# Optimization experiments

Measured on AMD Instinct MI355X. Metric: run time of the kernel, lower is better.

## Reference

```python
import jax, jax.numpy as jnp
import numpy as np

SEQ_LEN = 2048
D_MODEL = 1024
K = 32
B = 16
CP = K * (K + 1) // 2  # 528


def _spectral_filters(seq_len: int, k: int) -> np.ndarray:
    # Hankel matrix Z_ij = 2 / ((i+j)^3 - (i+j)), 1-indexed
    e = np.arange(1, seq_len + 1, dtype=np.float64)
    ipj = e[:, None] + e[None, :]
    Z = 2.0 / (ipj ** 3 - ipj)
    sigma, phi = np.linalg.eigh(Z)
    sk = np.clip(sigma[-k:], 1e-9, None)
    return (phi[:, -k:] * sk ** 0.25).astype(np.float32)


# static upper-triangular index pattern and sqrt(2) off-diagonal scaling
_IU0, _IU1 = np.triu_indices(K)
_SCALE = np.where(_IU0 == _IU1, 1.0, np.sqrt(2.0)).astype(np.float32)


def setup_inputs() -> dict:
    key = jax.random.key(0)
    ks = jax.random.split(key, 8)
    filters = jnp.asarray(_spectral_filters(SEQ_LEN, K))
    x = jax.random.normal(ks[0], (B, SEQ_LEN, D_MODEL), dtype=jnp.float32)
    pre_w = jax.random.normal(ks[1], (SEQ_LEN, D_MODEL), dtype=jnp.float32) / np.sqrt(D_MODEL)
    pre_b = jnp.zeros((SEQ_LEN,), dtype=jnp.float32)
    qp_w = jax.random.normal(ks[2], (CP, K), dtype=jnp.float32) / np.sqrt(K)
    qp_b = jnp.zeros((CP,), dtype=jnp.float32)
    o_w = jax.random.normal(ks[3], (D_MODEL, CP), dtype=jnp.float32) / np.sqrt(CP)
    o_b = jnp.zeros((D_MODEL,), dtype=jnp.float32)
    decay = jnp.ones((SEQ_LEN,), dtype=jnp.float32)
    return {
        'x': x,
        'pre_w': pre_w, 'pre_b': pre_b,
        'q_filters': filters,          # learnable copy
        'k_filters': filters,          # fixed buffer copy
        'qp_w': qp_w, 'qp_b': qp_b,
        'o_w': o_w, 'o_b': o_b,
        'decay': decay,
    }


def reference(x, pre_w, pre_b, q_filters, k_filters, qp_w, qp_b, o_w, o_b, decay):
    # pre_proj: (B,T,d_model) -> (B,T,seq_len)
    x_proj = x @ pre_w.T + pre_b
    # spectral projections onto top-K filters: (B,T,K)
    Q = jnp.einsum('bti,ik->btk', x_proj, q_filters)
    Q = Q @ qp_w.T + qp_b                      # (B,T,CP)
    V = jnp.einsum('bti,ik->btk', x_proj, k_filters)
    # symmetric outer product compressed to upper triangle, off-diag * sqrt(2)
    iu0 = jnp.asarray(_IU0)
    iu1 = jnp.asarray(_IU1)
    scale = jnp.asarray(_SCALE)
    Z = V[..., iu0] * V[..., iu1] * scale      # (B,T,CP), avoids (B,T,K,K)
    Z = Z * decay[None, :, None]
    H = jnp.cumsum(Z, axis=1)                  # causal state accumulation
    Y = Q * H
    return Y @ o_w.T + o_b                     # (B,T,d_model)
```

## Files before the change

### kernel.cpp

```cpp
#include <hip/hip_runtime.h>
#include <hip/hip_bf16.h>
#include <math.h>

#define T_SEQ   2048
#define DM      1024
#define KF      32
#define BATCH   16
#define CPDIM   528
#define KPAD    576
#define MROWS   (BATCH * T_SEQ)
#define NCHUNK  32
#define TCHUNK  64

typedef __bf16 bf16x8 __attribute__((ext_vector_type(8)));
typedef float f32x4 __attribute__((ext_vector_type(4)));
typedef unsigned uint2v __attribute__((ext_vector_type(2)));

__device__ __forceinline__ unsigned packsplit(float v) {
  unsigned u = __float_as_uint(v);
  unsigned h = (u + 0x7fffu + ((u >> 16) & 1u)) & 0xffff0000u;
  float rr = v - __uint_as_float(h);
  return h | (__float_as_uint(rr) >> 16);
}

__device__ __forceinline__ unsigned short f2bf(float f) {
  unsigned u = __float_as_uint(f);
  return (unsigned short)((u + 0x7fffu + ((u >> 16) & 1u)) >> 16);
}

__device__ __forceinline__ void gload16(const void* g, void* l) {
  __builtin_amdgcn_global_load_lds(
      (const __attribute__((address_space(1))) unsigned*)g,
      (__attribute__((address_space(3))) unsigned*)l, 16, 0, 0);
}

__global__ __launch_bounds__(256) void k_fold_part(const float* __restrict__ pre_w,
                                                   const float* __restrict__ qf,
                                                   const float* __restrict__ kfil,
                                                   float* __restrict__ Wp) {
  const int sc = blockIdx.x;
  const int it = blockIdx.y;
  const int s0 = sc * 64, i0 = it * 64;
  const int tid = threadIdx.x;
  __shared__ float fs[64][64];
  __shared__ float ps[64][64];
  for (int idx = tid; idx < 4096; idx += 256) {
    const int s = idx >> 6, c = idx & 63;
    fs[s][c] = (c < KF) ? qf[(s0 + s) * KF + c] : kfil[(s0 + s) * KF + c - KF];
    ps[s][c] = pre_w[(size_t)(s0 + s) * DM + i0 + c];
  }
  __syncthreads();
  const int i = tid & 63;
  const int kb = tid >> 6;
  float acc[16] = {};
  for (int s = 0; s < 64; ++s) {
    const float pv = ps[s][i];
    const float4 f0 = *reinterpret_cast<const float4*>(&fs[s][kb * 16 + 0]);
    const float4 f1 = *reinterpret_cast<const float4*>(&fs[s][kb * 16 + 4]);
    const float4 f2 = *reinterpret_cast<const float4*>(&fs[s][kb * 16 + 8]);
    const float4 f3 = *reinterpret_cast<const float4*>(&fs[s][kb * 16 + 12]);
    acc[0]  = fmaf(pv, f0.x, acc[0]);  acc[1]  = fmaf(pv, f0.y, acc[1]);
    acc[2]  = fmaf(pv, f0.z, acc[2]);  acc[3]  = fmaf(pv, f0.w, acc[3]);
    acc[4]  = fmaf(pv, f1.x, acc[4]);  acc[5]  = fmaf(pv, f1.y, acc[5]);
    acc[6]  = fmaf(pv, f1.z, acc[6]);  acc[7]  = fmaf(pv, f1.w, acc[7]);
    acc[8]  = fmaf(pv, f2.x, acc[8]);  acc[9]  = fmaf(pv, f2.y, acc[9]);
    acc[10] = fmaf(pv, f2.z, acc[10]); acc[11] = fmaf(pv, f2.w, acc[11]);
    acc[12] = fmaf(pv, f3.x, acc[12]); acc[13] = fmaf(pv, f3.y, acc[13]);
    acc[14] = fmaf(pv, f3.z, acc[14]); acc[15] = fmaf(pv, f3.w, acc[15]);
  }
#pragma unroll
  for (int j = 0; j < 16; ++j)
    Wp[((size_t)sc * 64 + kb * 16 + j) * DM + i0 + i] = acc[j];
}

__global__ __launch_bounds__(256) void k_foldred(const float* __restrict__ Wp,
                                                 unsigned short* __restrict__ Wt_hi,
                                                 unsigned short* __restrict__ Wt_lo) {
  const int idx = blockIdx.x * 256 + threadIdx.x;
  float acc = 0.f;
#pragma unroll
  for (int sc = 0; sc < NCHUNK; ++sc)
    acc += Wp[(size_t)sc * 64 * DM + idx];
  const unsigned pk = packsplit(acc);
  Wt_hi[idx] = (unsigned short)(pk >> 16);
  Wt_lo[idx] = (unsigned short)(pk & 0xffffu);
}

__global__ __launch_bounds__(256) void k_bias(const float* __restrict__ pre_b,
                                              const float* __restrict__ qf,
                                              const float* __restrict__ kfil,
                                              float* __restrict__ bias64) {
  __shared__ float part[4][64];
  const int k = threadIdx.x & 63;
  const int q = threadIdx.x >> 6;
  float acc = 0.f;
  for (int s = q * 512; s < (q + 1) * 512; ++s) {
    const float fv = (k < KF) ? qf[s * KF + k] : kfil[s * KF + k - KF];
    acc = fmaf(pre_b[s], fv, acc);
  }
  part[q][k] = acc;
  __syncthreads();
  if (threadIdx.x < 64)
    bias64[threadIdx.x] = part[0][k] + part[1][k] + part[2][k] + part[3][k];
}

__global__ __launch_bounds__(256) void k_q0v(const float* __restrict__ x,
                                             const unsigned short* __restrict__ Wt_hi,
                                             const unsigned short* __restrict__ Wt_lo,
                                             const float* __restrict__ bias64,
                                             float* __restrict__ Q0V) {
  __shared__ float Xs[2][64 * 32];
  __shared__ unsigned short Wh[2][64 * 32];
  __shared__ unsigned short Wl[2][64 * 32];
  const int tid = threadIdx.x;
  const int m0 = blockIdx.x * 64;
  const int w = tid >> 6, l = tid & 63;
  const int g = l >> 4, r = l & 15;

  f32x4 acc[4] = {};

  auto stage = [&](int buf, int k0) {
#pragma unroll
    for (int q = 0; q < 2; ++q) {
      const int c = q * 256 + tid;
      const int row = c >> 3, sl = c & 7;
      const int col4 = (sl ^ (row & 7)) * 4;
      gload16(&x[(size_t)(m0 + row) * DM + k0 + col4], &Xs[buf][c * 4]);
    }
    {
      const int row = tid >> 2, sl = tid & 3;
      const int colh = (sl ^ ((row >> 1) & 3)) * 8;
      gload16(&Wt_hi[(size_t)row * DM + k0 + colh], &Wh[buf][tid * 8]);
      gload16(&Wt_lo[(size_t)row * DM + k0 + colh], &Wl[buf][tid * 8]);
    }
  };

  stage(0, 0);
  for (int it = 0; it < DM / 32; ++it) {
    const int cur = it & 1;
    __syncthreads();
    if (it + 1 < DM / 32) stage(cur ^ 1, (it + 1) * 32);

    const int arow = w * 16 + r;
    const int sx = (2 * g) ^ (arow & 7);
    const int sy = (2 * g + 1) ^ (arow & 7);
    const f32x4 pX = *reinterpret_cast<const f32x4*>(&Xs[cur][arow * 32 + sx * 4]);
    const f32x4 pY = *reinterpret_cast<const f32x4*>(&Xs[cur][arow * 32 + sy * 4]);
    unsigned pk[8];
#pragma unroll
    for (int e = 0; e < 4; ++e) { pk[e] = packsplit(pX[e]); pk[4 + e] = packsplit(pY[e]); }
    union { unsigned u[4]; bf16x8 v; } ah, al;
#pragma unroll
    for (int j = 0; j < 4; ++j) {
      ah.u[j] = (pk[2 * j] >> 16) | (pk[2 * j + 1] & 0xffff0000u);
      al.u[j] = (pk[2 * j] & 0xffffu) | (pk[2 * j + 1] << 16);
    }

    bf16x8 bh[4], bl[4];
#pragma unroll
    for (int n = 0; n < 4; ++n) {
      const int brow = n * 16 + r;
      const int bs = g ^ ((brow >> 1) & 3);
      const int off = brow * 32 + bs * 8;
      bh[n] = *reinterpret_cast<const bf16x8*>(&Wh[cur][off]);
      bl[n] = *reinterpret_cast<const bf16x8*>(&Wl[cur][off]);
    }
#pragma unroll
    for (int n = 0; n < 4; ++n) {
      acc[n] = __builtin_amdgcn_mfma_f32_16x16x32_bf16(bh[n], ah.v, acc[n], 0, 0, 0);
      acc[n] = __builtin_amdgcn_mfma_f32_16x16x32_bf16(bh[n], al.v, acc[n], 0, 0, 0);
      acc[n] = __builtin_amdgcn_mfma_f32_16x16x32_bf16(bl[n], ah.v, acc[n], 0, 0, 0);
    }
  }
  const int row_o = m0 + w * 16 + r;
#pragma unroll
  for (int n = 0; n < 4; ++n) {
    const int col_o = n * 16 + g * 4;
    const float4 bb = *reinterpret_cast<const float4*>(&bias64[col_o]);
    float4 v;
    v.x = acc[n][0] + bb.x; v.y = acc[n][1] + bb.y;
    v.z = acc[n][2] + bb.z; v.w = acc[n][3] + bb.w;
    *reinterpret_cast<float4*>(&Q0V[(size_t)row_o * 64 + col_o]) = v;
  }
}

__global__ __launch_bounds__(576) void k_chunksum(const float* __restrict__ Q0V,
                                                  const float* __restrict__ decay,
                                                  float* __restrict__ S) {
  const int ch = blockIdx.x;
  const int b  = blockIdx.y;
  __shared__ float vs[TCHUNK * KF];
  __shared__ float dec[TCHUNK];
  const int tid = threadIdx.x;
  const int t0 = ch * TCHUNK;

  for (int idx = tid; idx < TCHUNK * KF; idx += 576) {
    const int t = idx >> 5, j = idx & 31;
    vs[idx] = Q0V[(size_t)(b * T_SEQ + t0 + t) * 64 + KF + j];
  }
  if (tid < TCHUNK) dec[tid] = decay[t0 + tid];
  __syncthreads();

  if (tid >= CPDIM) return;
  const int c = tid;
  int i = 0, rem = c;
  while (rem >= KF - i) { rem -= KF - i; ++i; }
  const int j = i + rem;
  const float sc = (i == j) ? 1.0f : 1.41421356237309515f;
  float h = 0.f;
#pragma unroll 4
  for (int t = 0; t < TCHUNK; ++t)
    h = fmaf(vs[t * KF + i] * vs[t * KF + j], dec[t], h);
  S[(size_t)(b * NCHUNK + ch) * CPDIM + c] = h * sc;
}

__global__ __launch_bounds__(576) void k_scanchunks(float* __restrict__ S) {
  const int b = blockIdx.x;
  const int c = threadIdx.x;
  if (c >= CPDIM) return;
  float v[NCHUNK];
#pragma unroll
  for (int ch = 0; ch < NCHUNK; ++ch)
    v[ch] = S[(size_t)(b * NCHUNK + ch) * CPDIM + c];
  float run = 0.f;
#pragma unroll
  for (int ch = 0; ch < NCHUNK; ++ch) {
    S[(size_t)(b * NCHUNK + ch) * CPDIM + c] = run;
    run += v[ch];
  }
}

__global__ __launch_bounds__(576) void k_scan_y(const float* __restrict__ Q0V,
                                                const float* __restrict__ S,
                                                const float* __restrict__ qp_w,
                                                const float* __restrict__ qp_b,
                                                const float* __restrict__ decay,
                                                unsigned short* __restrict__ Yb) {
  const int ch = blockIdx.x;
  const int b  = blockIdx.y;
  __shared__ float vs[TCHUNK * KF];
  __shared__ float qs[TCHUNK * KF];
  __shared__ float dec[TCHUNK];
  const int tid = threadIdx.x;
  const int t0 = ch * TCHUNK;

  for (int idx = tid; idx < TCHUNK * KF; idx += 576) {
    const int t = idx >> 5, j = idx & 31;
    const size_t row = (size_t)(b * T_SEQ + t0 + t) * 64;
    qs[idx] = Q0V[row + j];
    vs[idx] = Q0V[row + KF + j];
  }
  if (tid < TCHUNK) dec[tid] = decay[t0 + tid];
  __syncthreads();

  const int c = tid;
  if (c >= CPDIM) {
    for (int t = 0; t < TCHUNK; ++t)
      Yb[(size_t)(b * T_SEQ + t0 + t) * KPAD + c] = 0;
    return;
  }
  int i = 0, rem = c;
  while (rem >= KF - i) { rem -= KF - i; ++i; }
  const int j = i + rem;
  const float sc = (i == j) ? 1.0f : 1.41421356237309515f;

  float w[KF];
#pragma unroll
  for (int q = 0; q < KF; ++q) w[q] = qp_w[c * KF + q];
  const float qb = qp_b[c];

  float h = S[(size_t)(b * NCHUNK + ch) * CPDIM + c];
  for (int t = 0; t < TCHUNK; ++t) {
    const float z = vs[t * KF + i] * vs[t * KF + j] * sc * dec[t];
    h += z;
    float qv = qb;
#pragma unroll
    for (int q = 0; q < KF; ++q) qv = fmaf(w[q], qs[t * KF + q], qv);
    Yb[(size_t)(b * T_SEQ + t0 + t) * KPAD + c] = f2bf(qv * h);
  }
}

__global__ __launch_bounds__(256) void k_owb(const float* __restrict__ ow,
                                             unsigned short* __restrict__ owb) {
  const int idx = blockIdx.x * 256 + threadIdx.x;
  if (idx >= DM * KPAD) return;
  const int n = idx / KPAD, k = idx - n * KPAD;
  owb[idx] = (k < CPDIM) ? f2bf(ow[(size_t)n * CPDIM + k]) : (unsigned short)0;
}

__global__ __launch_bounds__(256) void k_out_mfma(const unsigned short* __restrict__ Yb,
                                                  const unsigned short* __restrict__ owb,
                                                  const float* __restrict__ ob,
                                                  float* __restrict__ out) {
  __shared__ unsigned short As[128 * 64];
  __shared__ unsigned short Bs[128 * 64];

  const int wg = blockIdx.x;
  const int nb = (wg & 7) * 256 + (wg >> 3);
  const int m0 = (nb >> 3) * 128;
  const int n0 = (nb & 7) * 128;

  const int tid = threadIdx.x;
  const int w = tid >> 6, l = tid & 63;
  const int wr = w >> 1, wc = w & 1;
  const int g = l >> 4, r = l & 15;

  f32x4 acc[4][4] = {};

  auto stage = [&](int k0) {
#pragma unroll
    for (int i = 0; i < 4; ++i) {
      const int c = i * 256 + tid;
      const int row = c >> 3, colh = (c & 7) * 8;
      gload16(&Yb [(size_t)(m0 + row) * KPAD + k0 + colh], &As[c * 8]);
      gload16(&owb[(size_t)(n0 + row) * KPAD + k0 + colh], &Bs[c * 8]);
    }
  };

  stage(0);
  for (int it = 0; it < KPAD / 64; ++it) {
    __syncthreads();

#pragma unroll
    for (int ksub = 0; ksub < 2; ++ksub) {
      bf16x8 af[4], bf[4];
      const int kh = ksub * 32 + g * 8;
#pragma unroll
      for (int m = 0; m < 4; ++m)
        af[m] = *reinterpret_cast<const bf16x8*>(&As[(wr * 64 + m * 16 + r) * 64 + kh]);
#pragma unroll
      for (int n = 0; n < 4; ++n)
        bf[n] = *reinterpret_cast<const bf16x8*>(&Bs[(wc * 64 + n * 16 + r) * 64 + kh]);
#pragma unroll
      for (int m = 0; m < 4; ++m)
#pragma unroll
        for (int n = 0; n < 4; ++n)
          acc[m][n] = __builtin_amdgcn_mfma_f32_16x16x32_bf16(bf[n], af[m], acc[m][n], 0, 0, 0);
    }

    __syncthreads();
    if (it + 1 < KPAD / 64) stage((it + 1) * 64);
  }

#pragma unroll
  for (int m = 0; m < 4; ++m) {
    const int row_o = m0 + wr * 64 + m * 16 + r;
#pragma unroll
    for (int n = 0; n < 4; ++n) {
      const int col_o = n0 + wc * 64 + n * 16 + g * 4;
      const float4 bb = *reinterpret_cast<const float4*>(&ob[col_o]);
      float4 v;
      v.x = acc[m][n][0] + bb.x; v.y = acc[m][n][1] + bb.y;
      v.z = acc[m][n][2] + bb.z; v.w = acc[m][n][3] + bb.w;
      *reinterpret_cast<float4*>(&out[(size_t)row_o * DM + col_o]) = v;
    }
  }
}

extern "C" void kernel_launch(void* const* d_in, const int* in_sizes, int n_in,
                              void* d_out, int out_size, void* d_ws, size_t ws_size,
                              hipStream_t stream) {
  const float* x      = (const float*)d_in[0];
  const float* pre_w  = (const float*)d_in[1];
  const float* pre_b  = (const float*)d_in[2];
  const float* q_filt = (const float*)d_in[3];
  const float* k_filt = (const float*)d_in[4];
  const float* qp_w   = (const float*)d_in[5];
  const float* qp_b   = (const float*)d_in[6];
  const float* o_w    = (const float*)d_in[7];
  const float* o_b    = (const float*)d_in[8];
  const float* decay  = (const float*)d_in[9];
  float* out = (float*)d_out;

  char* ws = (char*)d_ws;
  unsigned short* Wt_hi = (unsigned short*)(ws);
  unsigned short* Wt_lo = (unsigned short*)(ws + 131072);
  float*    bias64 = (float*)(ws + 262144);
  float*    Q0V    = (float*)(ws + 262400);
  unsigned short* owb = (unsigned short*)(ws + 262400);
  float*    S      = (float*)(ws + 8651008);
  unsigned short* Yb = (unsigned short*)(ws + 9732352);
  float*    Wp     = (float*)(ws + 50331648);

  k_fold_part<<<dim3(NCHUNK, 16), dim3(256), 0, stream>>>(pre_w, q_filt, k_filt, Wp);
  k_foldred<<<dim3(256), dim3(256), 0, stream>>>(Wp, Wt_hi, Wt_lo);
  k_bias<<<dim3(1), dim3(256), 0, stream>>>(pre_b, q_filt, k_filt, bias64);
  k_q0v<<<dim3(MROWS / 64), dim3(256), 0, stream>>>(x, Wt_hi, Wt_lo, bias64, Q0V);
  k_chunksum<<<dim3(NCHUNK, BATCH), dim3(576), 0, stream>>>(Q0V, decay, S);
  k_scanchunks<<<dim3(BATCH), dim3(576), 0, stream>>>(S);
  k_scan_y<<<dim3(NCHUNK, BATCH), dim3(576), 0, stream>>>(Q0V, S, qp_w, qp_b, decay, Yb);
  k_owb<<<dim3((DM * KPAD + 255) / 256), dim3(256), 0, stream>>>(o_w, owb);
  k_out_mfma<<<dim3((MROWS / 128) * (DM / 128)), dim3(256), 0, stream>>>(Yb, owb, o_b, out);
}
```

Before: 205.2 us.

## Fuse chunk sums into Q0V GEMM and scan_y into output GEMM via LDS

Merges the bias reduction into the fold-reduce kernel and computes per-chunk state sums inside the Q0V projection kernel from values already in registers. It also fuses the intra-chunk scan and Y computation into the output GEMM: each 64-row block builds its bf16 Y tile in LDS (padded stride) and multiplies it by o_w fragments loaded straight from global memory into registers with double buffering. This removes the global Yb round trip and several launches, and trims the K padding from 576 to 544. In exchange the output GEMM block covers the full 1024-wide N with large register accumulators and reads B from global memory without LDS staging, which may hurt occupancy and bandwidth.

Result: slower. 219.9 us (+7.2%).

```diff
diff --git a/kernel.cpp b/kernel.cpp
--- a/kernel.cpp
+++ b/kernel.cpp
@@ -7,7 +7,8 @@
 #define KF      32
 #define BATCH   16
 #define CPDIM   528
-#define KPAD    576
+#define KPAD    544
+#define YSTR    552
 #define MROWS   (BATCH * T_SEQ)
 #define NCHUNK  32
 #define TCHUNK  64
@@ -73,9 +74,28 @@
     Wp[((size_t)sc * 64 + kb * 16 + j) * DM + i0 + i] = acc[j];
 }
 
-__global__ __launch_bounds__(256) void k_foldred(const float* __restrict__ Wp,
-                                                 unsigned short* __restrict__ Wt_hi,
-                                                 unsigned short* __restrict__ Wt_lo) {
+__global__ __launch_bounds__(256) void k_foldred_bias(const float* __restrict__ Wp,
+                                                      const float* __restrict__ pre_b,
+                                                      const float* __restrict__ qf,
+                                                      const float* __restrict__ kfil,
+                                                      unsigned short* __restrict__ Wt_hi,
+                                                      unsigned short* __restrict__ Wt_lo,
+                                                      float* __restrict__ bias64) {
+  if (blockIdx.x == 256) {
+    __shared__ float part[4][64];
+    const int k = threadIdx.x & 63;
+    const int q = threadIdx.x >> 6;
+    float acc = 0.f;
+    for (int s = q * 512; s < (q + 1) * 512; ++s) {
+      const float fv = (k < KF) ? qf[s * KF + k] : kfil[s * KF + k - KF];
+      acc = fmaf(pre_b[s], fv, acc);
+    }
+    part[q][k] = acc;
+    __syncthreads();
+    if (threadIdx.x < 64)
+      bias64[threadIdx.x] = part[0][k] + part[1][k] + part[2][k] + part[3][k];
+    return;
+  }
   const int idx = blockIdx.x * 256 + threadIdx.x;
   float acc = 0.f;
 #pragma unroll
@@ -86,32 +106,18 @@
   Wt_lo[idx] = (unsigned short)(pk & 0xffffu);
 }
 
-__global__ __launch_bounds__(256) void k_bias(const float* __restrict__ pre_b,
-                                              const float* __restrict__ qf,
-                                              const float* __restrict__ kfil,
-                                              float* __restrict__ bias64) {
-  __shared__ float part[4][64];
-  const int k = threadIdx.x & 63;
-  const int q = threadIdx.x >> 6;
-  float acc = 0.f;
-  for (int s = q * 512; s < (q + 1) * 512; ++s) {
-    const float fv = (k < KF) ? qf[s * KF + k] : kfil[s * KF + k - KF];
-    acc = fmaf(pre_b[s], fv, acc);
-  }
-  part[q][k] = acc;
-  __syncthreads();
-  if (threadIdx.x < 64)
-    bias64[threadIdx.x] = part[0][k] + part[1][k] + part[2][k] + part[3][k];
-}
-
-__global__ __launch_bounds__(256) void k_q0v(const float* __restrict__ x,
-                                             const unsigned short* __restrict__ Wt_hi,
-                                             const unsigned short* __restrict__ Wt_lo,
-                                             const float* __restrict__ bias64,
-                                             float* __restrict__ Q0V) {
+__global__ __launch_bounds__(256) void k_q0v_cs(const float* __restrict__ x,
+                                                const unsigned short* __restrict__ Wt_hi,
+                                                const unsigned short* __restrict__ Wt_lo,
+                                                const float* __restrict__ bias64,
+                                                const float* __restrict__ decay,
+                                                float* __restrict__ Q0V,
+                                                float* __restrict__ S) {
   __shared__ float Xs[2][64 * 32];
   __shared__ unsigned short Wh[2][64 * 32];
   __shared__ unsigned short Wl[2][64 * 32];
+  __shared__ float vs2[64 * 32];
+  __shared__ float dec2[64];
   const int tid = threadIdx.x;
   const int m0 = blockIdx.x * 64;
   const int w = tid >> 6, l = tid & 63;
@@ -134,6 +140,8 @@
       gload16(&Wt_lo[(size_t)row * DM + k0 + colh], &Wl[buf][tid * 8]);
     }
   };
+
+  if (tid < 64) dec2[tid] = decay[(m0 & 2047) + tid];
 
   stage(0, 0);
   for (int it = 0; it < DM / 32; ++it) {
@@ -172,7 +180,9 @@
       acc[n] = __builtin_amdgcn_mfma_f32_16x16x32_bf16(bl[n], ah.v, acc[n], 0, 0, 0);
     }
   }
-  const int row_o = m0 + w * 16 + r;
+
+  const int trow = w * 16 + r;
+  const int row_o = m0 + trow;
 #pragma unroll
   for (int n = 0; n < 4; ++n) {
     const int col_o = n * 16 + g * 4;
@@ -181,37 +191,27 @@
     v.x = acc[n][0] + bb.x; v.y = acc[n][1] + bb.y;
     v.z = acc[n][2] + bb.z; v.w = acc[n][3] + bb.w;
     *reinterpret_cast<float4*>(&Q0V[(size_t)row_o * 64 + col_o]) = v;
-  }
-}
-
-__global__ __launch_bounds__(576) void k_chunksum(const float* __restrict__ Q0V,
-                                                  const float* __restrict__ decay,
-                                                  float* __restrict__ S) {
-  const int ch = blockIdx.x;
-  const int b  = blockIdx.y;
-  __shared__ float vs[TCHUNK * KF];
-  __shared__ float dec[TCHUNK];
-  const int tid = threadIdx.x;
-  const int t0 = ch * TCHUNK;
-
-  for (int idx = tid; idx < TCHUNK * KF; idx += 576) {
-    const int t = idx >> 5, j = idx & 31;
-    vs[idx] = Q0V[(size_t)(b * T_SEQ + t0 + t) * 64 + KF + j];
-  }
-  if (tid < TCHUNK) dec[tid] = decay[t0 + tid];
+    if (n >= 2)
+      *reinterpret_cast<float4*>(&vs2[trow * 32 + (n - 2) * 16 + g * 4]) = v;
+  }
   __syncthreads();
 
-  if (tid >= CPDIM) return;
-  const int c = tid;
-  int i = 0, rem = c;
-  while (rem >= KF - i) { rem -= KF - i; ++i; }
-  const int j = i + rem;
-  const float sc = (i == j) ? 1.0f : 1.41421356237309515f;
-  float h = 0.f;
+  const int b = m0 >> 11, ch = (m0 & 2047) >> 6;
+#pragma unroll
+  for (int pass = 0; pass < 3; ++pass) {
+    const int c = tid + pass * 256;
+    if (c < CPDIM) {
+      int i = 0, rem = c;
+      while (rem >= KF - i) { rem -= KF - i; ++i; }
+      const int j = i + rem;
+      const float sc = (i == j) ? 1.0f : 1.41421356237309515f;
+      float h = 0.f;
 #pragma unroll 4
-  for (int t = 0; t < TCHUNK; ++t)
-    h = fmaf(vs[t * KF + i] * vs[t * KF + j], dec[t], h);
-  S[(size_t)(b * NCHUNK + ch) * CPDIM + c] = h * sc;
+      for (int t = 0; t < TCHUNK; ++t)
+        h = fmaf(vs2[t * KF + i] * vs2[t * KF + j], dec2[t], h);
+      S[(size_t)(b * NCHUNK + ch) * CPDIM + c] = h * sc;
+    }
+  }
 }
 
 __global__ __launch_bounds__(576) void k_scanchunks(float* __restrict__ S) {
@@ -230,124 +230,110 @@
   }
 }
 
-__global__ __launch_bounds__(576) void k_scan_y(const float* __restrict__ Q0V,
-                                                const float* __restrict__ S,
-                                                const float* __restrict__ qp_w,
-                                                const float* __restrict__ qp_b,
-                                                const float* __restrict__ decay,
-                                                unsigned short* __restrict__ Yb) {
-  const int ch = blockIdx.x;
-  const int b  = blockIdx.y;
-  __shared__ float vs[TCHUNK * KF];
-  __shared__ float qs[TCHUNK * KF];
-  __shared__ float dec[TCHUNK];
-  const int tid = threadIdx.x;
-  const int t0 = ch * TCHUNK;
-
-  for (int idx = tid; idx < TCHUNK * KF; idx += 576) {
-    const int t = idx >> 5, j = idx & 31;
-    const size_t row = (size_t)(b * T_SEQ + t0 + t) * 64;
-    qs[idx] = Q0V[row + j];
-    vs[idx] = Q0V[row + KF + j];
-  }
-  if (tid < TCHUNK) dec[tid] = decay[t0 + tid];
-  __syncthreads();
-
-  const int c = tid;
-  if (c >= CPDIM) {
-    for (int t = 0; t < TCHUNK; ++t)
-      Yb[(size_t)(b * T_SEQ + t0 + t) * KPAD + c] = 0;
-    return;
-  }
-  int i = 0, rem = c;
-  while (rem >= KF - i) { rem -= KF - i; ++i; }
-  const int j = i + rem;
-  const float sc = (i == j) ? 1.0f : 1.41421356237309515f;
-
-  float w[KF];
-#pragma unroll
-  for (int q = 0; q < KF; ++q) w[q] = qp_w[c * KF + q];
-  const float qb = qp_b[c];
-
-  float h = S[(size_t)(b * NCHUNK + ch) * CPDIM + c];
-  for (int t = 0; t < TCHUNK; ++t) {
-    const float z = vs[t * KF + i] * vs[t * KF + j] * sc * dec[t];
-    h += z;
-    float qv = qb;
-#pragma unroll
-    for (int q = 0; q < KF; ++q) qv = fmaf(w[q], qs[t * KF + q], qv);
-    Yb[(size_t)(b * T_SEQ + t0 + t) * KPAD + c] = f2bf(qv * h);
-  }
-}
-
-__global__ __launch_bounds__(256) void k_owb(const float* __restrict__ ow,
-                                             unsigned short* __restrict__ owb) {
+__global__ __launch_bounds__(256) void k_prep(const float* __restrict__ ow,
+                                              unsigned short* __restrict__ owb) {
   const int idx = blockIdx.x * 256 + threadIdx.x;
   if (idx >= DM * KPAD) return;
   const int n = idx / KPAD, k = idx - n * KPAD;
   owb[idx] = (k < CPDIM) ? f2bf(ow[(size_t)n * CPDIM + k]) : (unsigned short)0;
 }
 
-__global__ __launch_bounds__(256) void k_out_mfma(const unsigned short* __restrict__ Yb,
-                                                  const unsigned short* __restrict__ owb,
-                                                  const float* __restrict__ ob,
-                                                  float* __restrict__ out) {
-  __shared__ unsigned short As[128 * 64];
-  __shared__ unsigned short Bs[128 * 64];
-
-  const int wg = blockIdx.x;
-  const int nb = (wg & 7) * 256 + (wg >> 3);
-  const int m0 = (nb >> 3) * 128;
-  const int n0 = (nb & 7) * 128;
-
+__global__ __launch_bounds__(512, 2) void k_out_fused(const float* __restrict__ Q0V,
+                                                      const float* __restrict__ S,
+                                                      const float* __restrict__ qp_w,
+                                                      const float* __restrict__ qp_b,
+                                                      const float* __restrict__ decay,
+                                                      const unsigned short* __restrict__ owb,
+                                                      const float* __restrict__ ob,
+                                                      float* __restrict__ out) {
+  __shared__ float qs[64 * 32];
+  __shared__ float vs[64 * 32];
+  __shared__ float dec[64];
+  __shared__ unsigned short Ylds[64 * YSTR];
   const int tid = threadIdx.x;
-  const int w = tid >> 6, l = tid & 63;
-  const int wr = w >> 1, wc = w & 1;
+  const int m0 = blockIdx.x * 64;
+  const int b = m0 >> 11, ch = (m0 & 2047) >> 6;
+  const int t0 = m0 & 2047;
+
+#pragma unroll
+  for (int ii = 0; ii < 2; ++ii) {
+    const int idx = ii * 512 + tid;
+    const int row = idx >> 4, c4 = idx & 15;
+    const float4 v = *reinterpret_cast<const float4*>(&Q0V[(size_t)(m0 + row) * 64 + c4 * 4]);
+    float* dst = (c4 < 8) ? &qs[row * 32 + c4 * 4] : &vs[row * 32 + (c4 - 8) * 4];
+    *reinterpret_cast<float4*>(dst) = v;
+  }
+  if (tid < 64) dec[tid] = decay[t0 + tid];
+  __syncthreads();
+
+#pragma unroll
+  for (int pass = 0; pass < 2; ++pass) {
+    const int c = tid + pass * 512;
+    if (c < CPDIM) {
+      int i = 0, rem = c;
+      while (rem >= KF - i) { rem -= KF - i; ++i; }
+      const int j = i + rem;
+      const float sc = (i == j) ? 1.0f : 1.41421356237309515f;
+      float wt[KF];
+#pragma unroll
+      for (int q = 0; q < KF; ++q) wt[q] = qp_w[c * KF + q];
+      const float qb = qp_b[c];
+      float h = S[(size_t)(b * NCHUNK + ch) * CPDIM + c];
+      for (int t = 0; t < TCHUNK; ++t) {
+        const float z = vs[t * KF + i] * vs[t * KF + j] * sc * dec[t];
+        h += z;
+        float qv = qb;
+#pragma unroll
+        for (int q = 0; q < KF; ++q) qv = fmaf(wt[q], qs[t * KF + q], qv);
+        Ylds[t * YSTR + c] = f2bf(qv * h);
+      }
+    }
+  }
+  if (tid >= 16 && tid < 32) {
+    for (int t = 0; t < TCHUNK; ++t)
+      Ylds[t * YSTR + 512 + tid] = 0;
+  }
+  __syncthreads();
+
+  const int wv = tid >> 6, l = tid & 63;
   const int g = l >> 4, r = l & 15;
-
-  f32x4 acc[4][4] = {};
-
-  auto stage = [&](int k0) {
-#pragma unroll
-    for (int i = 0; i < 4; ++i) {
-      const int c = i * 256 + tid;
-      const int row = c >> 3, colh = (c & 7) * 8;
-      gload16(&Yb [(size_t)(m0 + row) * KPAD + k0 + colh], &As[c * 8]);
-      gload16(&owb[(size_t)(n0 + row) * KPAD + k0 + colh], &Bs[c * 8]);
-    }
+  f32x4 acc[4][8] = {};
+  bf16x8 bA[8], bB[8];
+
+  auto loadB = [&](bf16x8 (&dst)[8], int ks) {
+    const int kh = ks * 32 + g * 8;
+#pragma unroll
+    for (int n = 0; n < 8; ++n)
+      dst[n] = *reinterpret_cast<const bf16x8*>(&owb[(size_t)(wv * 128 + n * 16 + r) * KPAD + kh]);
   };
-
-  stage(0);
-  for (int it = 0; it < KPAD / 64; ++it) {
-    __syncthreads();
-
-#pragma unroll
-    for (int ksub = 0; ksub < 2; ++ksub) {
-      bf16x8 af[4], bf[4];
-      const int kh = ksub * 32 + g * 8;
-#pragma unroll
-      for (int m = 0; m < 4; ++m)
-        af[m] = *reinterpret_cast<const bf16x8*>(&As[(wr * 64 + m * 16 + r) * 64 + kh]);
-#pragma unroll
-      for (int n = 0; n < 4; ++n)
-        bf[n] = *reinterpret_cast<const bf16x8*>(&Bs[(wc * 64 + n * 16 + r) * 64 + kh]);
-#pragma unroll
-      for (int m = 0; m < 4; ++m)
-#pragma unroll
-        for (int n = 0; n < 4; ++n)
-          acc[m][n] = __builtin_amdgcn_mfma_f32_16x16x32_bf16(bf[n], af[m], acc[m][n], 0, 0, 0);
-    }
-
-    __syncthreads();
-    if (it + 1 < KPAD / 64) stage((it + 1) * 64);
-  }
+  auto step = [&](bf16x8 (&bcur)[8], int ks) {
+    const int kh = ks * 32 + g * 8;
+    bf16x8 af[4];
+#pragma unroll
+    for (int m = 0; m < 4; ++m)
+      af[m] = *reinterpret_cast<const bf16x8*>(&Ylds[(m * 16 + r) * YSTR + kh]);
+#pragma unroll
+    for (int m = 0; m < 4; ++m)
+#pragma unroll
+      for (int n = 0; n < 8; ++n)
+        acc[m][n] = __builtin_amdgcn_mfma_f32_16x16x32_bf16(bcur[n], af[m], acc[m][n], 0, 0, 0);
+  };
+
+  loadB(bA, 0);
+  for (int ks = 0; ks < 16; ks += 2) {
+    loadB(bB, ks + 1);
+    step(bA, ks);
+    loadB(bA, ks + 2);
+    step(bB, ks + 1);
+  }
+  step(bA, 16);
 
 #pragma unroll
   for (int m = 0; m < 4; ++m) {
-    const int row_o = m0 + wr * 64 + m * 16 + r;
-#pragma unroll
-    for (int n = 0; n < 4; ++n) {
-      const int col_o = n0 + wc * 64 + n * 16 + g * 4;
+    const int row_o = m0 + m * 16 + r;
+#pragma unroll
+    for (int n = 0; n < 8; ++n) {
+      const int col_o = wv * 128 + n * 16 + g * 4;
       const float4 bb = *reinterpret_cast<const float4*>(&ob[col_o]);
       float4 v;
       v.x = acc[m][n][0] + bb.x; v.y = acc[m][n][1] + bb.y;
@@ -377,18 +363,14 @@
   unsigned short* Wt_lo = (unsigned short*)(ws + 131072);
   float*    bias64 = (float*)(ws + 262144);
   float*    Q0V    = (float*)(ws + 262400);
-  unsigned short* owb = (unsigned short*)(ws + 262400);
   float*    S      = (float*)(ws + 8651008);
-  unsigned short* Yb = (unsigned short*)(ws + 9732352);
-  float*    Wp     = (float*)(ws + 50331648);
+  unsigned short* owb = (unsigned short*)(ws + 9732352);
+  float*    Wp     = (float*)(ws + 16777216);
 
   k_fold_part<<<dim3(NCHUNK, 16), dim3(256), 0, stream>>>(pre_w, q_filt, k_filt, Wp);
-  k_foldred<<<dim3(256), dim3(256), 0, stream>>>(Wp, Wt_hi, Wt_lo);
-  k_bias<<<dim3(1), dim3(256), 0, stream>>>(pre_b, q_filt, k_filt, bias64);
-  k_q0v<<<dim3(MROWS / 64), dim3(256), 0, stream>>>(x, Wt_hi, Wt_lo, bias64, Q0V);
-  k_chunksum<<<dim3(NCHUNK, BATCH), dim3(576), 0, stream>>>(Q0V, decay, S);
+  k_foldred_bias<<<dim3(257), dim3(256), 0, stream>>>(Wp, pre_b, q_filt, k_filt, Wt_hi, Wt_lo, bias64);
+  k_q0v_cs<<<dim3(MROWS / 64), dim3(256), 0, stream>>>(x, Wt_hi, Wt_lo, bias64, decay, Q0V, S);
   k_scanchunks<<<dim3(BATCH), dim3(576), 0, stream>>>(S);
-  k_scan_y<<<dim3(NCHUNK, BATCH), dim3(576), 0, stream>>>(Q0V, S, qp_w, qp_b, decay, Yb);
-  k_owb<<<dim3((DM * KPAD + 255) / 256), dim3(256), 0, stream>>>(o_w, owb);
-  k_out_mfma<<<dim3((MROWS / 128) * (DM / 128)), dim3(256), 0, stream>>>(Yb, owb, o_b, out);
-}
+  k_prep<<<dim3((DM * KPAD + 255) / 256), dim3(256), 0, stream>>>(o_w, owb);
+  k_out_fused<<<dim3(MROWS / 64), dim3(512), 0, stream>>>(Q0V, S, qp_w, qp_b, decay, owb, o_b, out);
+}
```

## Fuse chunk-sum into Q0V GEMM, triple-buffer loads, merge bias into fold reduction

Applied to the files above, without the earlier changes.

Merges the bias kernel into the fold-reduce kernel as an extra block. Fuses the per-chunk outer-product sum into the Q0V projection kernel so the V values are consumed from shared memory instead of being re-read from global memory. The projection kernel moves to 512 threads, with the N dimension split across wave pairs, and to a three-stage global-to-LDS pipeline that uses explicit vmcnt waits and raw barriers. Workspace offsets are rearranged, and the fused kernel holds more LDS and carries the chunk-sum tail in every block.

Result: faster. 199.0 us (-3.0%).

```diff
diff --git a/kernel.cpp b/kernel.cpp
--- a/kernel.cpp
+++ b/kernel.cpp
@@ -14,7 +14,6 @@
 
 typedef __bf16 bf16x8 __attribute__((ext_vector_type(8)));
 typedef float f32x4 __attribute__((ext_vector_type(4)));
-typedef unsigned uint2v __attribute__((ext_vector_type(2)));
 
 __device__ __forceinline__ unsigned packsplit(float v) {
   unsigned u = __float_as_uint(v);
@@ -73,9 +72,28 @@
     Wp[((size_t)sc * 64 + kb * 16 + j) * DM + i0 + i] = acc[j];
 }
 
-__global__ __launch_bounds__(256) void k_foldred(const float* __restrict__ Wp,
-                                                 unsigned short* __restrict__ Wt_hi,
-                                                 unsigned short* __restrict__ Wt_lo) {
+__global__ __launch_bounds__(256) void k_foldred_bias(const float* __restrict__ Wp,
+                                                      const float* __restrict__ pre_b,
+                                                      const float* __restrict__ qf,
+                                                      const float* __restrict__ kfil,
+                                                      unsigned short* __restrict__ Wt_hi,
+                                                      unsigned short* __restrict__ Wt_lo,
+                                                      float* __restrict__ bias64) {
+  if (blockIdx.x == 256) {
+    __shared__ float part[4][64];
+    const int k = threadIdx.x & 63;
+    const int q = threadIdx.x >> 6;
+    float acc = 0.f;
+    for (int s = q * 512; s < (q + 1) * 512; ++s) {
+      const float fv = (k < KF) ? qf[s * KF + k] : kfil[s * KF + k - KF];
+      acc = fmaf(pre_b[s], fv, acc);
+    }
+    part[q][k] = acc;
+    __syncthreads();
+    if (threadIdx.x < 64)
+      bias64[threadIdx.x] = part[0][k] + part[1][k] + part[2][k] + part[3][k];
+    return;
+  }
   const int idx = blockIdx.x * 256 + threadIdx.x;
   float acc = 0.f;
 #pragma unroll
@@ -86,62 +104,45 @@
   Wt_lo[idx] = (unsigned short)(pk & 0xffffu);
 }
 
-__global__ __launch_bounds__(256) void k_bias(const float* __restrict__ pre_b,
-                                              const float* __restrict__ qf,
-                                              const float* __restrict__ kfil,
-                                              float* __restrict__ bias64) {
-  __shared__ float part[4][64];
-  const int k = threadIdx.x & 63;
-  const int q = threadIdx.x >> 6;
-  float acc = 0.f;
-  for (int s = q * 512; s < (q + 1) * 512; ++s) {
-    const float fv = (k < KF) ? qf[s * KF + k] : kfil[s * KF + k - KF];
-    acc = fmaf(pre_b[s], fv, acc);
-  }
-  part[q][k] = acc;
-  __syncthreads();
-  if (threadIdx.x < 64)
-    bias64[threadIdx.x] = part[0][k] + part[1][k] + part[2][k] + part[3][k];
-}
-
-__global__ __launch_bounds__(256) void k_q0v(const float* __restrict__ x,
-                                             const unsigned short* __restrict__ Wt_hi,
-                                             const unsigned short* __restrict__ Wt_lo,
-                                             const float* __restrict__ bias64,
-                                             float* __restrict__ Q0V) {
-  __shared__ float Xs[2][64 * 32];
-  __shared__ unsigned short Wh[2][64 * 32];
-  __shared__ unsigned short Wl[2][64 * 32];
+__global__ __launch_bounds__(512) void k_q0v_cs(const float* __restrict__ x,
+                                                const unsigned short* __restrict__ Wt_hi,
+                                                const unsigned short* __restrict__ Wt_lo,
+                                                const float* __restrict__ bias64,
+                                                const float* __restrict__ decay,
+                                                float* __restrict__ Q0V,
+                                                float* __restrict__ S) {
+  __shared__ float Xs[3][64 * 32];
+  __shared__ unsigned short Wh[3][64 * 32];
+  __shared__ unsigned short Wl[3][64 * 32];
+  __shared__ float vs2[64 * 32];
+  __shared__ float dec2[64];
   const int tid = threadIdx.x;
   const int m0 = blockIdx.x * 64;
   const int w = tid >> 6, l = tid & 63;
   const int g = l >> 4, r = l & 15;
-
-  f32x4 acc[4] = {};
+  const int wr = w & 3, wh = w >> 2;
+
+  f32x4 acc[2] = {};
 
   auto stage = [&](int buf, int k0) {
-#pragma unroll
-    for (int q = 0; q < 2; ++q) {
-      const int c = q * 256 + tid;
-      const int row = c >> 3, sl = c & 7;
+    {
+      const int row = tid >> 3, sl = tid & 7;
       const int col4 = (sl ^ (row & 7)) * 4;
-      gload16(&x[(size_t)(m0 + row) * DM + k0 + col4], &Xs[buf][c * 4]);
+      gload16(&x[(size_t)(m0 + row) * DM + k0 + col4], &Xs[buf][tid * 4]);
     }
     {
-      const int row = tid >> 2, sl = tid & 3;
+      const int c2 = tid & 255;
+      const int row = c2 >> 2, sl = c2 & 3;
       const int colh = (sl ^ ((row >> 1) & 3)) * 8;
-      gload16(&Wt_hi[(size_t)row * DM + k0 + colh], &Wh[buf][tid * 8]);
-      gload16(&Wt_lo[(size_t)row * DM + k0 + colh], &Wl[buf][tid * 8]);
+      unsigned short* dst = (tid < 256) ? &Wh[buf][c2 * 8] : &Wl[buf][c2 * 8];
+      const unsigned short* src = (tid < 256) ? &Wt_hi[(size_t)row * DM + k0 + colh]
+                                              : &Wt_lo[(size_t)row * DM + k0 + colh];
+      gload16(src, dst);
     }
   };
 
-  stage(0, 0);
-  for (int it = 0; it < DM / 32; ++it) {
-    const int cur = it & 1;
-    __syncthreads();
-    if (it + 1 < DM / 32) stage(cur ^ 1, (it + 1) * 32);
-
-    const int arow = w * 16 + r;
+  auto compute = [&](int cur) {
+    const int arow = wr * 16 + r;
     const int sx = (2 * g) ^ (arow & 7);
     const int sy = (2 * g + 1) ^ (arow & 7);
     const f32x4 pX = *reinterpret_cast<const f32x4*>(&Xs[cur][arow * 32 + sx * 4]);
@@ -155,63 +156,80 @@
       ah.u[j] = (pk[2 * j] >> 16) | (pk[2 * j + 1] & 0xffff0000u);
       al.u[j] = (pk[2 * j] & 0xffffu) | (pk[2 * j + 1] << 16);
     }
-
-    bf16x8 bh[4], bl[4];
-#pragma unroll
-    for (int n = 0; n < 4; ++n) {
-      const int brow = n * 16 + r;
+    bf16x8 bh[2], bl[2];
+#pragma unroll
+    for (int nb = 0; nb < 2; ++nb) {
+      const int brow = (wh * 2 + nb) * 16 + r;
       const int bs = g ^ ((brow >> 1) & 3);
       const int off = brow * 32 + bs * 8;
-      bh[n] = *reinterpret_cast<const bf16x8*>(&Wh[cur][off]);
-      bl[n] = *reinterpret_cast<const bf16x8*>(&Wl[cur][off]);
-    }
-#pragma unroll
-    for (int n = 0; n < 4; ++n) {
-      acc[n] = __builtin_amdgcn_mfma_f32_16x16x32_bf16(bh[n], ah.v, acc[n], 0, 0, 0);
-      acc[n] = __builtin_amdgcn_mfma_f32_16x16x32_bf16(bh[n], al.v, acc[n], 0, 0, 0);
-      acc[n] = __builtin_amdgcn_mfma_f32_16x16x32_bf16(bl[n], ah.v, acc[n], 0, 0, 0);
-    }
-  }
-  const int row_o = m0 + w * 16 + r;
-#pragma unroll
-  for (int n = 0; n < 4; ++n) {
+      bh[nb] = *reinterpret_cast<const bf16x8*>(&Wh[cur][off]);
+      bl[nb] = *reinterpret_cast<const bf16x8*>(&Wl[cur][off]);
+    }
+#pragma unroll
+    for (int nb = 0; nb < 2; ++nb) {
+      acc[nb] = __builtin_amdgcn_mfma_f32_16x16x32_bf16(bh[nb], ah.v, acc[nb], 0, 0, 0);
+      acc[nb] = __builtin_amdgcn_mfma_f32_16x16x32_bf16(bh[nb], al.v, acc[nb], 0, 0, 0);
+      acc[nb] = __builtin_amdgcn_mfma_f32_16x16x32_bf16(bl[nb], ah.v, acc[nb], 0, 0, 0);
+    }
+  };
+
+  if (tid < 64) dec2[tid] = decay[(m0 & 2047) + tid];
+
+  stage(0, 0);
+  stage(1, 32);
+
+  for (int base = 0; base < 30; base += 3) {
+#pragma unroll
+    for (int sub = 0; sub < 3; ++sub) {
+      const int it = base + sub;
+      asm volatile("s_waitcnt vmcnt(2)" ::: "memory");
+      __builtin_amdgcn_s_barrier();
+      __builtin_amdgcn_sched_barrier(0);
+      stage((sub + 2) % 3, (it + 2) * 32);
+      compute(sub);
+    }
+  }
+  asm volatile("s_waitcnt vmcnt(2)" ::: "memory");
+  __builtin_amdgcn_s_barrier();
+  __builtin_amdgcn_sched_barrier(0);
+  compute(0);
+  asm volatile("s_waitcnt vmcnt(0)" ::: "memory");
+  __builtin_amdgcn_s_barrier();
+  __builtin_amdgcn_sched_barrier(0);
+  compute(1);
+
+  const int trow = wr * 16 + r;
+  const int row_o = m0 + trow;
+#pragma unroll
+  for (int nb = 0; nb < 2; ++nb) {
+    const int n = wh * 2 + nb;
     const int col_o = n * 16 + g * 4;
     const float4 bb = *reinterpret_cast<const float4*>(&bias64[col_o]);
     float4 v;
-    v.x = acc[n][0] + bb.x; v.y = acc[n][1] + bb.y;
-    v.z = acc[n][2] + bb.z; v.w = acc[n][3] + bb.w;
+    v.x = acc[nb][0] + bb.x; v.y = acc[nb][1] + bb.y;
+    v.z = acc[nb][2] + bb.z; v.w = acc[nb][3] + bb.w;
     *reinterpret_cast<float4*>(&Q0V[(size_t)row_o * 64 + col_o]) = v;
-  }
-}
-
-__global__ __launch_bounds__(576) void k_chunksum(const float* __restrict__ Q0V,
-                                                  const float* __restrict__ decay,
-                                                  float* __restrict__ S) {
-  const int ch = blockIdx.x;
-  const int b  = blockIdx.y;
-  __shared__ float vs[TCHUNK * KF];
-  __shared__ float dec[TCHUNK];
-  const int tid = threadIdx.x;
-  const int t0 = ch * TCHUNK;
-
-  for (int idx = tid; idx < TCHUNK * KF; idx += 576) {
-    const int t = idx >> 5, j = idx & 31;
-    vs[idx] = Q0V[(size_t)(b * T_SEQ + t0 + t) * 64 + KF + j];
-  }
-  if (tid < TCHUNK) dec[tid] = decay[t0 + tid];
+    if (n >= 2)
+      *reinterpret_cast<float4*>(&vs2[trow * 32 + (n - 2) * 16 + g * 4]) = v;
+  }
   __syncthreads();
 
-  if (tid >= CPDIM) return;
-  const int c = tid;
-  int i = 0, rem = c;
-  while (rem >= KF - i) { rem -= KF - i; ++i; }
-  const int j = i + rem;
-  const float sc = (i == j) ? 1.0f : 1.41421356237309515f;
-  float h = 0.f;
+  const int b = m0 >> 11, ch = (m0 & 2047) >> 6;
+#pragma unroll
+  for (int pass = 0; pass < 2; ++pass) {
+    const int c = tid + pass * 512;
+    if (c < CPDIM) {
+      int i = 0, rem = c;
+      while (rem >= KF - i) { rem -= KF - i; ++i; }
+      const int j = i + rem;
+      const float sc = (i == j) ? 1.0f : 1.41421356237309515f;
+      float h = 0.f;
 #pragma unroll 4
-  for (int t = 0; t < TCHUNK; ++t)
-    h = fmaf(vs[t * KF + i] * vs[t * KF + j], dec[t], h);
-  S[(size_t)(b * NCHUNK + ch) * CPDIM + c] = h * sc;
+      for (int t = 0; t < TCHUNK; ++t)
+        h = fmaf(vs2[t * KF + i] * vs2[t * KF + j], dec2[t], h);
+      S[(size_t)(b * NCHUNK + ch) * CPDIM + c] = h * sc;
+    }
+  }
 }
 
 __global__ __launch_bounds__(576) void k_scanchunks(float* __restrict__ S) {
@@ -377,16 +395,14 @@
   unsigned short* Wt_lo = (unsigned short*)(ws + 131072);
   float*    bias64 = (float*)(ws + 262144);
   float*    Q0V    = (float*)(ws + 262400);
-  unsigned short* owb = (unsigned short*)(ws + 262400);
   float*    S      = (float*)(ws + 8651008);
-  unsigned short* Yb = (unsigned short*)(ws + 9732352);
-  float*    Wp     = (float*)(ws + 50331648);
+  unsigned short* owb = (unsigned short*)(ws + 9732352);
+  float*    Wp     = (float*)(ws + 16777216);
+  unsigned short* Yb = (unsigned short*)(ws + 25165824);
 
   k_fold_part<<<dim3(NCHUNK, 16), dim3(256), 0, stream>>>(pre_w, q_filt, k_filt, Wp);
-  k_foldred<<<dim3(256), dim3(256), 0, stream>>>(Wp, Wt_hi, Wt_lo);
-  k_bias<<<dim3(1), dim3(256), 0, stream>>>(pre_b, q_filt, k_filt, bias64);
-  k_q0v<<<dim3(MROWS / 64), dim3(256), 0, stream>>>(x, Wt_hi, Wt_lo, bias64, Q0V);
-  k_chunksum<<<dim3(NCHUNK, BATCH), dim3(576), 0, stream>>>(Q0V, decay, S);
+  k_foldred_bias<<<dim3(257), dim3(256), 0, stream>>>(Wp, pre_b, q_filt, k_filt, Wt_hi, Wt_lo, bias64);
+  k_q0v_cs<<<dim3(MROWS / 64), dim3(512), 0, stream>>>(x, Wt_hi, Wt_lo, bias64, decay, Q0V, S);
   k_scanchunks<<<dim3(BATCH), dim3(576), 0, stream>>>(S);
   k_scan_y<<<dim3(NCHUNK, BATCH), dim3(576), 0, stream>>>(Q0V, S, qp_w, qp_b, decay, Yb);
   k_owb<<<dim3((DM * KPAD + 255) / 256), dim3(256), 0, stream>>>(o_w, owb);
```
